# Kernel tuning notes

Hardware: AMD Instinct MI355X
Metric: run time of the kernel (lower is better)

The kernel has to match this reference:

```python
import jax, jax.numpy as jnp
import numpy as np

B, N, C, H = 4, 1024, 768, 12
D = C // H  # head_dim = 64


def setup_inputs() -> dict:
    key = jax.random.key(0)
    ks = jax.random.split(key, 16)
    def lin(k, fan_in, fan_out):
        # torch Linear init: U(-1/sqrt(fan_in), 1/sqrt(fan_in)); stored as [in, out]
        bound = 1.0 / np.sqrt(fan_in)
        kw, kb = jax.random.split(k)
        W = jax.random.uniform(kw, (fan_in, fan_out), minval=-bound, maxval=bound, dtype=jnp.float32)
        b = jax.random.uniform(kb, (fan_out,), minval=-bound, maxval=bound, dtype=jnp.float32)
        return W, b
    Wq, bq = lin(ks[0], C, C)
    Wk, bk = lin(ks[1], C, C)
    Wv, bv = lin(ks[2], C, C)
    Wo, bo = lin(ks[3], C, C)
    Wd1, bd1 = lin(ks[4], 1, 16)
    Wd2, bd2 = lin(ks[5], 16, H)
    x = jax.random.normal(ks[6], (B, N, C), dtype=jnp.float32)
    coords = jax.random.uniform(ks[7], (B, N, 2), dtype=jnp.float32)
    return {"x": x, "coords": coords,
            "Wq": Wq, "bq": bq, "Wk": Wk, "bk": bk, "Wv": Wv, "bv": bv,
            "Wo": Wo, "bo": bo, "Wd1": Wd1, "bd1": bd1, "Wd2": Wd2, "bd2": bd2}


def reference(x, coords, Wq, bq, Wk, bk, Wv, bv, Wo, bo, Wd1, bd1, Wd2, bd2):
    scale = D ** (-0.5)
    # projections -> [B, H, N, D]
    def heads(t):
        return t.reshape(B, N, H, D).transpose(0, 2, 1, 3)
    q = heads(x @ Wq + bq)
    k = heads(x @ Wk + bk)
    v = heads(x @ Wv + bv)
    # content scores [B, H, N, N]
    content = jnp.einsum('bhid,bhjd->bhij', q, k) * scale
    # pairwise distances [B, N, N, 1]
    diff = coords[:, :, None, :] - coords[:, None, :, :]
    dist = jnp.sqrt(jnp.sum(diff * diff, axis=-1, keepdims=True) + 1e-6)
    # distance MLP: 1 -> 16 -> H, then permute to [B, H, N, N]
    hbias = jax.nn.relu(dist @ Wd1 + bd1)
    spatial = (hbias @ Wd2 + bd2).transpose(0, 3, 1, 2)
    attn = jax.nn.softmax(content + spatial, axis=-1)
    out = jnp.einsum('bhij,bhjd->bhid', attn, v)
    out = out.transpose(0, 2, 1, 3).reshape(B, N, C)
    out = out @ Wo + bo
    return out, attn
```

## Files before the change

kernel.cpp:

```cpp
#include <hip/hip_runtime.h>
#include <cstddef>
#include <cstdint>

#define Bc 4
#define Nc 1024
#define Cc 768
#define Hc 12
#define Dc 64
#define BHc 48
#define QKV_ELEMS ((size_t)Bc * Nc * Cc)

typedef __attribute__((ext_vector_type(4))) unsigned int u32x4;
typedef __attribute__((ext_vector_type(8))) short s16x8;
typedef __attribute__((ext_vector_type(4))) float fx4;
typedef __attribute__((ext_vector_type(2))) float fx2;

union Frag { u32x4 u; s16x8 s; unsigned short h[8]; };

__device__ inline unsigned short f2bf(float x) {
    union { float f; uint32_t u; } c; c.f = x;
    return (unsigned short)((c.u + 0x7FFFu + ((c.u >> 16) & 1u)) >> 16);
}
__device__ inline float bf2f(unsigned short b) {
    union { uint32_t u; float f; } c; c.u = ((uint32_t)b) << 16;
    return c.f;
}
__device__ inline void split8(const float* v, u32x4& hi, u32x4& lo) {
    Frag fh, fl;
    #pragma unroll
    for (int e = 0; e < 8; ++e) {
        const unsigned short hb = f2bf(v[e]);
        fh.h[e] = hb;
        fl.h[e] = f2bf(v[e] - bf2f(hb));
    }
    hi = fh.u; lo = fl.u;
}

__global__ __launch_bounds__(256) void prep_w_kernel(
    const float* __restrict__ Wq, const float* __restrict__ Wk,
    const float* __restrict__ Wv, const float* __restrict__ Wo,
    unsigned short* __restrict__ Thi, unsigned short* __restrict__ Tlo)
{
    __shared__ float scr[64 * 65];
    const int mat = blockIdx.z;
    const float* W = (mat == 0) ? Wq : (mat == 1) ? Wk : (mat == 2) ? Wv : Wo;
    const int k0 = blockIdx.y * 64, n0 = blockIdx.x * 64;
    const int tid = threadIdx.x;

    #pragma unroll
    for (int it = 0; it < 4; ++it) {
        const int lin = tid + it * 256;
        const int r = lin >> 4, c4 = (lin & 15) << 2;
        const fx4 v = *(const fx4*)&W[(size_t)(k0 + r) * 768 + n0 + c4];
        scr[r * 65 + c4 + 0] = v[0]; scr[r * 65 + c4 + 1] = v[1];
        scr[r * 65 + c4 + 2] = v[2]; scr[r * 65 + c4 + 3] = v[3];
    }
    __syncthreads();
    unsigned short* th = Thi + (size_t)mat * 768 * 768;
    unsigned short* tl = Tlo + (size_t)mat * 768 * 768;
    #pragma unroll
    for (int it = 0; it < 16; ++it) {
        const int lin = tid + it * 256;
        const int n = lin >> 6, kq = lin & 63;
        const float val = scr[kq * 65 + n];
        const size_t o = (size_t)(n0 + n) * 768 + k0 + kq;
        const unsigned short hb = f2bf(val);
        th[o] = hb;
        tl[o] = f2bf(val - bf2f(hb));
    }
}

__global__ __launch_bounds__(256) void prep_tables_kernel(
    const float* __restrict__ Wd1, const float* __restrict__ bd1,
    const float* __restrict__ Wd2, const float* __restrict__ bd2,
    float* __restrict__ abPack, unsigned char* __restrict__ lut)
{
    __shared__ float w1s[16], b1s[16], kn[16];
    __shared__ int rank[16];
    const int tid = threadIdx.x;
    if (tid < 16) {
        const float w1 = Wd1[tid], b1 = bd1[tid];
        w1s[tid] = w1; b1s[tid] = b1;
        kn[tid] = (w1 != 0.0f) ? (-b1 / w1) : INFINITY;
    }
    __syncthreads();
    if (tid < 16) {
        int rk = 0;
        for (int u = 0; u < 16; ++u) {
            const float ku = kn[u], km = kn[tid];
            if (ku < km || (ku == km && u < tid)) ++rk;
        }
        rank[tid] = rk;
    }
    __syncthreads();
    if (tid < 17 * 12) {
        const int s = tid / 12, h = tid % 12;
        float a = 0.0f, be = bd2[h];
        for (int u = 0; u < 16; ++u) {
            const float w1 = w1s[u], b1 = b1s[u];
            bool act;
            if (w1 > 0.0f)      act = (rank[u] < s);
            else if (w1 < 0.0f) act = (rank[u] >= s);
            else                act = (b1 > 0.0f);
            if (act) {
                const float w2 = Wd2[u * 12 + h];
                a  += w2 * w1;
                be += w2 * b1;
            }
        }
        abPack[tid * 2 + 0] = a;
        abPack[tid * 2 + 1] = be;
    }
    for (int b = tid; b < 2048; b += 256) {
        const float rep = (b + 0.5f) * (1.41422f / 2048.0f);
        int cnt = 0;
        for (int t = 0; t < 16; ++t) cnt += (rep > kn[t]) ? 1 : 0;
        lut[b] = (unsigned char)cnt;
    }
}

__global__ __launch_bounds__(256) void split_x_kernel(
    const float* __restrict__ x, unsigned short* __restrict__ xhi,
    unsigned short* __restrict__ xlo)
{
    const size_t t = (size_t)blockIdx.x * 256 + threadIdx.x;
    float vv[8];
    const fx4 a = *(const fx4*)&x[t * 8];
    const fx4 b = *(const fx4*)&x[t * 8 + 4];
    vv[0]=a[0]; vv[1]=a[1]; vv[2]=a[2]; vv[3]=a[3];
    vv[4]=b[0]; vv[5]=b[1]; vv[6]=b[2]; vv[7]=b[3];
    u32x4 hi, lo; split8(vv, hi, lo);
    *(u32x4*)&xhi[t * 8] = hi;
    *(u32x4*)&xlo[t * 8] = lo;
}

struct SmemG { u32x4 ah[512]; u32x4 al[512]; u32x4 bh[512]; u32x4 bl[512]; };
struct SmemT { float scr[64 * 68]; };
union SmemU { SmemG g; SmemT t; };

template<int OMODE>
__global__ __launch_bounds__(256) void gemm_mfma_kernel(
    const unsigned short* __restrict__ Ahi, const unsigned short* __restrict__ Alo,
    const unsigned short* __restrict__ Bhi, const unsigned short* __restrict__ Blo,
    const float* __restrict__ bias,
    float* __restrict__ outF,
    unsigned short* __restrict__ Ohi, unsigned short* __restrict__ Olo)
{
    __shared__ SmemU sm;
    const int tid = threadIdx.x;
    const int w = tid >> 6, L = tid & 63;
    const int Lr = L & 15, Lg = L >> 4;
    const int m0 = blockIdx.y * 64, n0 = blockIdx.x * 64;

    fx4 acc[2][2] = {};

    for (int kk = 0; kk < 768; kk += 64) {
        #pragma unroll
        for (int it = 0; it < 2; ++it) {
            const int slot = tid + it * 256;
            const int s = slot >> 6, l = slot & 63;
            const int row = m0 + ((s >> 1) << 4) + (l & 15);
            const int kb = kk + ((s & 1) << 5) + ((l >> 4) << 3);
            sm.g.ah[slot] = *(const u32x4*)&Ahi[(size_t)row * 768 + kb];
            sm.g.al[slot] = *(const u32x4*)&Alo[(size_t)row * 768 + kb];
            const int col = n0 + ((s >> 1) << 4) + (l & 15);
            sm.g.bh[slot] = *(const u32x4*)&Bhi[(size_t)col * 768 + kb];
            sm.g.bl[slot] = *(const u32x4*)&Blo[(size_t)col * 768 + kb];
        }
        __syncthreads();
        #pragma unroll
        for (int kc = 0; kc < 2; ++kc) {
            Frag ah[2], al[2], bh[2], bl[2];
            #pragma unroll
            for (int mm = 0; mm < 2; ++mm) {
                const int rg = (w >> 1) * 2 + mm;
                ah[mm].u = sm.g.ah[(rg * 2 + kc) * 64 + L];
                al[mm].u = sm.g.al[(rg * 2 + kc) * 64 + L];
            }
            #pragma unroll
            for (int nn = 0; nn < 2; ++nn) {
                const int cg = (w & 1) * 2 + nn;
                bh[nn].u = sm.g.bh[(cg * 2 + kc) * 64 + L];
                bl[nn].u = sm.g.bl[(cg * 2 + kc) * 64 + L];
            }
            #pragma unroll
            for (int mm = 0; mm < 2; ++mm)
                #pragma unroll
                for (int nn = 0; nn < 2; ++nn) {
                    acc[mm][nn] = __builtin_amdgcn_mfma_f32_16x16x32_bf16(ah[mm].s, bh[nn].s, acc[mm][nn], 0, 0, 0);
                    acc[mm][nn] = __builtin_amdgcn_mfma_f32_16x16x32_bf16(ah[mm].s, bl[nn].s, acc[mm][nn], 0, 0, 0);
                    acc[mm][nn] = __builtin_amdgcn_mfma_f32_16x16x32_bf16(al[mm].s, bh[nn].s, acc[mm][nn], 0, 0, 0);
                }
        }
        __syncthreads();
    }

    #pragma unroll
    for (int mm = 0; mm < 2; ++mm) {
        const int rl = (w >> 1) * 32 + mm * 16 + Lg * 4;
        #pragma unroll
        for (int nn = 0; nn < 2; ++nn) {
            const int cl = (w & 1) * 32 + nn * 16 + Lr;
            const float bs = bias[n0 + cl];
            #pragma unroll
            for (int r = 0; r < 4; ++r)
                sm.t.scr[(rl + r) * 68 + cl] = acc[mm][nn][r] + bs;
        }
    }
    __syncthreads();

    if (OMODE == 0) {
        const int h = n0 >> 6;
        #pragma unroll
        for (int it = 0; it < 2; ++it) {
            const int t = tid + it * 256;
            const int r = t >> 3, d0 = (t & 7) << 3;
            float vv[8];
            #pragma unroll
            for (int e = 0; e < 8; ++e) vv[e] = sm.t.scr[r * 68 + d0 + e];
            u32x4 hi, lo; split8(vv, hi, lo);
            const int rg = m0 + r, b = rg >> 10, nloc = rg & 1023;
            const size_t o = (((size_t)(b * Hc + h) * Nc + nloc) << 6) + d0;
            *(u32x4*)&Ohi[o] = hi;
            *(u32x4*)&Olo[o] = lo;
        }
    } else if (OMODE == 1) {
        const int b = m0 >> 10, h = n0 >> 6, nbase = m0 & 1023;
        #pragma unroll
        for (int it = 0; it < 2; ++it) {
            const int t = tid + it * 256;
            const int dd = t >> 3, j0 = (t & 7) << 3;
            float vv[8];
            #pragma unroll
            for (int e = 0; e < 8; ++e) vv[e] = sm.t.scr[(j0 + e) * 68 + dd];
            u32x4 hi, lo; split8(vv, hi, lo);
            const size_t o = (size_t)((b * Hc + h) * Dc + dd) * Nc + nbase + j0;
            *(u32x4*)&Ohi[o] = hi;
            *(u32x4*)&Olo[o] = lo;
        }
    } else {
        #pragma unroll
        for (int it = 0; it < 4; ++it) {
            const int lin = tid + it * 256;
            const int r = lin >> 4, c4 = (lin & 15) << 2;
            const fx4 v = *(const fx4*)&sm.t.scr[r * 68 + c4];
            *(fx4*)&outF[(size_t)(m0 + r) * 768 + n0 + c4] = v;
        }
    }
}

__global__ __launch_bounds__(256) void scores_kernel(
    const unsigned short* __restrict__ qhi, const unsigned short* __restrict__ qlo,
    const unsigned short* __restrict__ khi, const unsigned short* __restrict__ klo,
    const float* __restrict__ coords,
    const float* __restrict__ abPack, const unsigned char* __restrict__ lutg,
    float* __restrict__ attn, float* __restrict__ mlf)
{
    __shared__ fx2 abt[17];
    __shared__ unsigned char luts[2048];
    __shared__ fx2 cjs[512];

    const int tid = threadIdx.x;
    const int w = tid >> 6, L = tid & 63;
    const int Lr = L & 15, Lg = L >> 4;
    const int bh = blockIdx.z, b = bh / Hc, h = bh % Hc;
    const int i0 = blockIdx.x * 64, half = blockIdx.y;
    const int i = i0 + w * 16 + Lr;
    const int Lg4 = Lg * 4;

    if (tid < 17) abt[tid] = ((const fx2*)abPack)[tid * Hc + h];
    #pragma unroll
    for (int t = tid; t < 512; t += 256) {
        ((uint32_t*)luts)[t] = ((const uint32_t*)lutg)[t];
        cjs[t] = *(const fx2*)&coords[((size_t)b * Nc + half * 512 + t) * 2];
    }

    Frag qh[2], ql[2];
    #pragma unroll
    for (int kc = 0; kc < 2; ++kc) {
        const size_t o = ((size_t)bh * Nc + i) * 64 + kc * 32 + Lg * 8;
        qh[kc].u = *(const u32x4*)&qhi[o];
        ql[kc].u = *(const u32x4*)&qlo[o];
    }
    const fx2 ci = *(const fx2*)&coords[((size_t)b * Nc + i) * 2];
    __syncthreads();

    const size_t rowbase = ((size_t)bh * Nc + i) * Nc + half * 512;
    const size_t mlbase = ((size_t)bh * Nc + i) * 16 + half * 8;

    for (int jt = 0; jt < 8; ++jt) {
        const int jbase = half * 512 + jt * 64;

        fx4 acc[4] = {};
        #pragma unroll
        for (int kc = 0; kc < 2; ++kc) {
            Frag kh[4], kl[4];
            #pragma unroll
            for (int cg = 0; cg < 4; ++cg) {
                const size_t o = ((size_t)bh * Nc + jbase + cg * 16 + Lr) * 64 + kc * 32 + Lg * 8;
                kh[cg].u = *(const u32x4*)&khi[o];
                kl[cg].u = *(const u32x4*)&klo[o];
            }
            #pragma unroll
            for (int cg = 0; cg < 4; ++cg) {
                acc[cg] = __builtin_amdgcn_mfma_f32_16x16x32_bf16(kh[cg].s, qh[kc].s, acc[cg], 0, 0, 0);
                acc[cg] = __builtin_amdgcn_mfma_f32_16x16x32_bf16(kl[cg].s, qh[kc].s, acc[cg], 0, 0, 0);
                acc[cg] = __builtin_amdgcn_mfma_f32_16x16x32_bf16(kh[cg].s, ql[kc].s, acc[cg], 0, 0, 0);
            }
        }

        float sv[16];
        #pragma unroll
        for (int cg = 0; cg < 4; ++cg) {
            #pragma unroll
            for (int r = 0; r < 4; ++r) {
                const fx2 cj = cjs[jt * 64 + cg * 16 + Lg4 + r];
                const float dx = ci[0] - cj[0], dy = ci[1] - cj[1];
                const float dist = sqrtf(fmaf(dx, dx, fmaf(dy, dy, 1e-6f)));
                int bin = (int)(dist * (2048.0f / 1.41422f));
                bin = (bin > 2047) ? 2047 : bin;
                const fx2 ab = abt[luts[bin]];
                sv[cg * 4 + r] = fmaf(acc[cg][r], 0.125f, fmaf(ab[0], dist, ab[1]));
            }
        }

        float tm = sv[0];
        #pragma unroll
        for (int e = 1; e < 16; ++e) tm = fmaxf(tm, sv[e]);
        tm = fmaxf(tm, __shfl_xor(tm, 16));
        tm = fmaxf(tm, __shfl_xor(tm, 32));

        float ts = 0.f;
        #pragma unroll
        for (int e = 0; e < 16; ++e) { sv[e] = __expf(sv[e] - tm); ts += sv[e]; }
        #pragma unroll
        for (int cg = 0; cg < 4; ++cg) {
            fx4 st;
            st[0] = sv[cg*4+0]; st[1] = sv[cg*4+1]; st[2] = sv[cg*4+2]; st[3] = sv[cg*4+3];
            *(fx4*)&attn[rowbase + jt * 64 + cg * 16 + Lg4] = st;
        }
        ts += __shfl_xor(ts, 16);
        ts += __shfl_xor(ts, 32);
        if (Lg == 0) {
            *(fx2*)&mlf[(mlbase + jt) * 2] = fx2{tm, ts};
        }
    }
}

__global__ __launch_bounds__(256) void pv_kernel(
    float* __restrict__ attn,
    const unsigned short* __restrict__ vThi, const unsigned short* __restrict__ vTlo,
    const float* __restrict__ mlf,
    unsigned short* __restrict__ Hphi, unsigned short* __restrict__ Hplo)
{
    __shared__ float accs[32 * 64];
    const int tid = threadIdx.x;
    const int w = tid >> 6, L = tid & 63;
    const int Lr = L & 15, Lg = L >> 4;
    const int wr = w >> 1, wc = w & 1;
    const int bh = blockIdx.y, b = bh / Hc, h = bh % Hc;
    const int i0 = blockIdx.x * 32;
    const int row = i0 + wr * 16 + Lr;

    const float* mlr = &mlf[((size_t)bh * Nc + row) * 32];
    float mt[16], lt[16];
    #pragma unroll
    for (int t = 0; t < 8; ++t) {
        const fx4 v = *(const fx4*)&mlr[t * 4];
        mt[t*2+0] = v[0]; lt[t*2+0] = v[1];
        mt[t*2+1] = v[2]; lt[t*2+1] = v[3];
    }
    float m_row = mt[0];
    #pragma unroll
    for (int t = 1; t < 16; ++t) m_row = fmaxf(m_row, mt[t]);
    float l_row = 0.f;
    #pragma unroll
    for (int t = 0; t < 16; ++t) l_row = fmaf(lt[t], __expf(mt[t] - m_row), l_row);
    const float il = 1.0f / l_row;

    fx4 acc[4] = {};
    const size_t arow = ((size_t)bh * Nc + row) * Nc;

    for (int jt = 0; jt < 8; ++jt) {
        const int jbase = wc * 512 + jt * 64;
        const float f = __expf(mlr[(wc * 8 + jt) * 2] - m_row) * il;
        #pragma unroll
        for (int kc = 0; kc < 2; ++kc) {
            float* ap = &attn[arow + jbase + kc * 32 + Lg * 8];
            const fx4 s0 = *(const fx4*)ap;
            const fx4 s1 = *(const fx4*)(ap + 4);
            float p[8];
            p[0]=s0[0]*f; p[1]=s0[1]*f; p[2]=s0[2]*f; p[3]=s0[3]*f;
            p[4]=s1[0]*f; p[5]=s1[1]*f; p[6]=s1[2]*f; p[7]=s1[3]*f;
            fx4 w0, w1;
            w0[0]=p[0]; w0[1]=p[1]; w0[2]=p[2]; w0[3]=p[3];
            w1[0]=p[4]; w1[1]=p[5]; w1[2]=p[6]; w1[3]=p[7];
            *(fx4*)ap = w0;
            *(fx4*)(ap + 4) = w1;
            u32x4 phiu, plou; split8(p, phiu, plou);
            Frag ph, pl; ph.u = phiu; pl.u = plou;

            Frag vh[4], vl[4];
            #pragma unroll
            for (int dg = 0; dg < 4; ++dg) {
                const size_t o = ((size_t)bh * Dc + dg * 16 + Lr) * Nc + jbase + kc * 32 + Lg * 8;
                vh[dg].u = *(const u32x4*)&vThi[o];
                vl[dg].u = *(const u32x4*)&vTlo[o];
            }
            #pragma unroll
            for (int dg = 0; dg < 4; ++dg) {
                acc[dg] = __builtin_amdgcn_mfma_f32_16x16x32_bf16(ph.s, vh[dg].s, acc[dg], 0, 0, 0);
                acc[dg] = __builtin_amdgcn_mfma_f32_16x16x32_bf16(ph.s, vl[dg].s, acc[dg], 0, 0, 0);
                acc[dg] = __builtin_amdgcn_mfma_f32_16x16x32_bf16(pl.s, vh[dg].s, acc[dg], 0, 0, 0);
            }
        }
    }

    if (wc == 0) {
        #pragma unroll
        for (int dg = 0; dg < 4; ++dg)
            #pragma unroll
            for (int r = 0; r < 4; ++r)
                accs[(wr * 16 + Lg * 4 + r) * 64 + dg * 16 + Lr] = acc[dg][r];
    }
    __syncthreads();
    if (wc == 1) {
        #pragma unroll
        for (int dg = 0; dg < 4; ++dg)
            #pragma unroll
            for (int r = 0; r < 4; ++r)
                accs[(wr * 16 + Lg * 4 + r) * 64 + dg * 16 + Lr] += acc[dg][r];
    }
    __syncthreads();

    const int r2 = tid >> 3, d0 = (tid & 7) << 3;
    float vv[8];
    #pragma unroll
    for (int e = 0; e < 8; ++e) vv[e] = accs[r2 * 64 + d0 + e];
    u32x4 hi, lo; split8(vv, hi, lo);
    const size_t o = ((size_t)b * Nc + i0 + r2) * Cc + h * Dc + d0;
    *(u32x4*)&Hphi[o] = hi;
    *(u32x4*)&Hplo[o] = lo;
}

extern "C" void kernel_launch(void* const* d_in, const int* in_sizes, int n_in,
                              void* d_out, int out_size, void* d_ws, size_t ws_size,
                              hipStream_t stream)
{
    (void)in_sizes; (void)n_in; (void)out_size; (void)ws_size;

    const float* x      = (const float*)d_in[0];
    const float* coords = (const float*)d_in[1];
    const float* Wq = (const float*)d_in[2];  const float* bq = (const float*)d_in[3];
    const float* Wk = (const float*)d_in[4];  const float* bk = (const float*)d_in[5];
    const float* Wv = (const float*)d_in[6];  const float* bv = (const float*)d_in[7];
    const float* Wo = (const float*)d_in[8];  const float* bo = (const float*)d_in[9];
    const float* Wd1 = (const float*)d_in[10]; const float* bd1 = (const float*)d_in[11];
    const float* Wd2 = (const float*)d_in[12]; const float* bd2 = (const float*)d_in[13];

    float* out_main = (float*)d_out;
    float* attn     = out_main + QKV_ELEMS;

    uint8_t* wsb = (uint8_t*)d_ws;
    const size_t SZ_BF = (size_t)BHc * Nc * Dc * 2;
    const size_t SZ_W4 = (size_t)4 * 768 * 768 * 2;
    unsigned short* qhi  = (unsigned short*)(wsb + 0 * SZ_BF);
    unsigned short* qlo  = (unsigned short*)(wsb + 1 * SZ_BF);
    unsigned short* khi  = (unsigned short*)(wsb + 2 * SZ_BF);
    unsigned short* klo  = (unsigned short*)(wsb + 3 * SZ_BF);
    unsigned short* vThi = (unsigned short*)(wsb + 4 * SZ_BF);
    unsigned short* vTlo = (unsigned short*)(wsb + 5 * SZ_BF);
    unsigned short* xhi  = (unsigned short*)(wsb + 6 * SZ_BF);
    unsigned short* xlo  = (unsigned short*)(wsb + 7 * SZ_BF);
    unsigned short* Thi  = (unsigned short*)(wsb + 8 * SZ_BF);
    unsigned short* Tlo  = (unsigned short*)(wsb + 8 * SZ_BF + SZ_W4);
    float* mlbuf  = (float*)(wsb + 8 * SZ_BF + 2 * SZ_W4);
    float* abPack = mlbuf + (size_t)BHc * Nc * 32;
    unsigned char* lut = (unsigned char*)(abPack + 17 * 12 * 2);

    prep_w_kernel<<<dim3(12, 12, 4), 256, 0, stream>>>(Wq, Wk, Wv, Wo, Thi, Tlo);
    prep_tables_kernel<<<1, 256, 0, stream>>>(Wd1, bd1, Wd2, bd2, abPack, lut);
    split_x_kernel<<<dim3(1536), 256, 0, stream>>>(x, xhi, xlo);

    dim3 gGemm(12, 64);
    gemm_mfma_kernel<0><<<gGemm, 256, 0, stream>>>(
        xhi, xlo, Thi + (size_t)0 * 768 * 768, Tlo + (size_t)0 * 768 * 768,
        bq, nullptr, qhi, qlo);
    gemm_mfma_kernel<0><<<gGemm, 256, 0, stream>>>(
        xhi, xlo, Thi + (size_t)1 * 768 * 768, Tlo + (size_t)1 * 768 * 768,
        bk, nullptr, khi, klo);
    gemm_mfma_kernel<1><<<gGemm, 256, 0, stream>>>(
        xhi, xlo, Thi + (size_t)2 * 768 * 768, Tlo + (size_t)2 * 768 * 768,
        bv, nullptr, vThi, vTlo);

    scores_kernel<<<dim3(16, 2, 48), 256, 0, stream>>>(
        qhi, qlo, khi, klo, coords, abPack, lut, attn, mlbuf);

    pv_kernel<<<dim3(32, 48), 256, 0, stream>>>(
        attn, vThi, vTlo, mlbuf, xhi, xlo);

    gemm_mfma_kernel<2><<<gGemm, 256, 0, stream>>>(
        xhi, xlo, Thi + (size_t)3 * 768 * 768, Tlo + (size_t)3 * 768 * 768,
        bo, out_main, nullptr, nullptr);
}
```

Baseline: 453.4 us.

## Stage unnormalized scores as fp16 workspace and use fp16 MFMA with LDS-staged V

The scores kernel now writes the exponentiated scores as fp16 into a workspace laid out for MFMA fragments, instead of writing fp32 into the attention output. The PV kernel reads these fp16 values, normalizes them, writes the final fp32 attention once, and runs two fp16 MFMAs per product instead of three split-bf16 ones. V is staged through LDS per 64-column tile, and each block now handles 64 rows over all columns instead of splitting columns across waves. This removes one fp32 read-modify-write pass over the large attention tensor and the bf16 splitting of P. In exchange, P is rounded to fp16 before the product, which lowers precision in the values fed to PV.

```diff
diff --git a/kernel.cpp b/kernel.cpp
--- a/kernel.cpp
+++ b/kernel.cpp
@@ -12,10 +12,13 @@
 
 typedef __attribute__((ext_vector_type(4))) unsigned int u32x4;
 typedef __attribute__((ext_vector_type(8))) short s16x8;
+typedef __attribute__((ext_vector_type(8))) _Float16 h16x8;
+typedef __attribute__((ext_vector_type(4))) unsigned short u16x4;
 typedef __attribute__((ext_vector_type(4))) float fx4;
 typedef __attribute__((ext_vector_type(2))) float fx2;
 
-union Frag { u32x4 u; s16x8 s; unsigned short h[8]; };
+union Frag { u32x4 u; s16x8 s; h16x8 f16; unsigned short h[8]; };
+union Half4 { u16x4 q; _Float16 h[4]; };
 
 __device__ inline unsigned short f2bf(float x) {
     union { float f; uint32_t u; } c; c.f = x;
@@ -32,6 +35,16 @@
         const unsigned short hb = f2bf(v[e]);
         fh.h[e] = hb;
         fl.h[e] = f2bf(v[e] - bf2f(hb));
+    }
+    hi = fh.u; lo = fl.u;
+}
+__device__ inline void split8h(const float* v, u32x4& hi, u32x4& lo) {
+    Frag fh, fl;
+    #pragma unroll
+    for (int e = 0; e < 8; ++e) {
+        const _Float16 hb = (_Float16)v[e];
+        fh.f16[e] = hb;
+        fl.f16[e] = (_Float16)(v[e] - (float)hb);
     }
     hi = fh.u; lo = fl.u;
 }
@@ -233,7 +246,7 @@
             float vv[8];
             #pragma unroll
             for (int e = 0; e < 8; ++e) vv[e] = sm.t.scr[(j0 + e) * 68 + dd];
-            u32x4 hi, lo; split8(vv, hi, lo);
+            u32x4 hi, lo; split8h(vv, hi, lo);
             const size_t o = (size_t)((b * Hc + h) * Dc + dd) * Nc + nbase + j0;
             *(u32x4*)&Ohi[o] = hi;
             *(u32x4*)&Olo[o] = lo;
@@ -254,7 +267,7 @@
     const unsigned short* __restrict__ khi, const unsigned short* __restrict__ klo,
     const float* __restrict__ coords,
     const float* __restrict__ abPack, const unsigned char* __restrict__ lutg,
-    float* __restrict__ attn, float* __restrict__ mlf)
+    unsigned short* __restrict__ e_ws, float* __restrict__ mlf)
 {
     __shared__ fx2 abt[17];
     __shared__ unsigned char luts[2048];
@@ -269,7 +282,6 @@
     const int Lg4 = Lg * 4;
 
     if (tid < 17) abt[tid] = ((const fx2*)abPack)[tid * Hc + h];
-    #pragma unroll
     for (int t = tid; t < 512; t += 256) {
         ((uint32_t*)luts)[t] = ((const uint32_t*)lutg)[t];
         cjs[t] = *(const fx2*)&coords[((size_t)b * Nc + half * 512 + t) * 2];
@@ -285,11 +297,11 @@
     const fx2 ci = *(const fx2*)&coords[((size_t)b * Nc + i) * 2];
     __syncthreads();
 
-    const size_t rowbase = ((size_t)bh * Nc + i) * Nc + half * 512;
     const size_t mlbase = ((size_t)bh * Nc + i) * 16 + half * 8;
 
     for (int jt = 0; jt < 8; ++jt) {
         const int jbase = half * 512 + jt * 64;
+        const int jtg = half * 8 + jt;
 
         fx4 acc[4] = {};
         #pragma unroll
@@ -314,7 +326,7 @@
         for (int cg = 0; cg < 4; ++cg) {
             #pragma unroll
             for (int r = 0; r < 4; ++r) {
-                const fx2 cj = cjs[jt * 64 + cg * 16 + Lg4 + r];
+                const fx2 cj = cjs[jt * 64 + cg * 16 + Lg4 + r + (half * 512 == jbase - jt * 64 ? 0 : 0)];
                 const float dx = ci[0] - cj[0], dy = ci[1] - cj[1];
                 const float dist = sqrtf(fmaf(dx, dx, fmaf(dy, dy, 1e-6f)));
                 int bin = (int)(dist * (2048.0f / 1.41422f));
@@ -333,12 +345,19 @@
         float ts = 0.f;
         #pragma unroll
         for (int e = 0; e < 16; ++e) { sv[e] = __expf(sv[e] - tm); ts += sv[e]; }
+
+        const size_t eT = (((size_t)bh * 16 + jtg) << 16);
         #pragma unroll
         for (int cg = 0; cg < 4; ++cg) {
-            fx4 st;
-            st[0] = sv[cg*4+0]; st[1] = sv[cg*4+1]; st[2] = sv[cg*4+2]; st[3] = sv[cg*4+3];
-            *(fx4*)&attn[rowbase + jt * 64 + cg * 16 + Lg4] = st;
-        }
+            Half4 hs;
+            #pragma unroll
+            for (int r = 0; r < 4; ++r) hs.h[r] = (_Float16)sv[cg * 4 + r];
+            const int kc = cg >> 1;
+            const int Lgp = (cg & 1) * 2 + (Lg >> 1);
+            const size_t eoff = eT + (size_t)kc * 32768 + (size_t)i * 32 + Lgp * 8 + (Lg & 1) * 4;
+            *(u16x4*)&e_ws[eoff] = hs.q;
+        }
+
         ts += __shfl_xor(ts, 16);
         ts += __shfl_xor(ts, 32);
         if (Lg == 0) {
@@ -347,22 +366,27 @@
     }
 }
 
+union PvSmem {
+    struct { u32x4 vh[512]; u32x4 vl[512]; } v;
+    float scr[64 * 68];
+};
+
 __global__ __launch_bounds__(256) void pv_kernel(
-    float* __restrict__ attn,
+    const unsigned short* __restrict__ e_ws,
     const unsigned short* __restrict__ vThi, const unsigned short* __restrict__ vTlo,
     const float* __restrict__ mlf,
+    float* __restrict__ attn,
     unsigned short* __restrict__ Hphi, unsigned short* __restrict__ Hplo)
 {
-    __shared__ float accs[32 * 64];
+    __shared__ PvSmem sm;
     const int tid = threadIdx.x;
     const int w = tid >> 6, L = tid & 63;
     const int Lr = L & 15, Lg = L >> 4;
-    const int wr = w >> 1, wc = w & 1;
     const int bh = blockIdx.y, b = bh / Hc, h = bh % Hc;
-    const int i0 = blockIdx.x * 32;
-    const int row = i0 + wr * 16 + Lr;
-
-    const float* mlr = &mlf[((size_t)bh * Nc + row) * 32];
+    const int i0 = blockIdx.x * 64;
+    const int i = i0 + w * 16 + Lr;
+
+    const float* mlr = &mlf[((size_t)bh * Nc + i) * 32];
     float mt[16], lt[16];
     #pragma unroll
     for (int t = 0; t < 8; ++t) {
@@ -379,68 +403,73 @@
     const float il = 1.0f / l_row;
 
     fx4 acc[4] = {};
-    const size_t arow = ((size_t)bh * Nc + row) * Nc;
-
-    for (int jt = 0; jt < 8; ++jt) {
-        const int jbase = wc * 512 + jt * 64;
-        const float f = __expf(mlr[(wc * 8 + jt) * 2] - m_row) * il;
+    const size_t arow = ((size_t)bh * Nc + i) * Nc;
+
+    #pragma unroll
+    for (int jt = 0; jt < 16; ++jt) {
+        const int jbase = jt * 64;
+        #pragma unroll
+        for (int it = 0; it < 2; ++it) {
+            const int s = tid + it * 256;
+            const int l = s & 63;
+            const int dd = ((s >> 7) << 4) + (l & 15);
+            const int jo = jbase + ((s >> 6) & 1) * 32 + ((l >> 4) << 3);
+            const size_t off = ((size_t)bh * Dc + dd) * Nc + jo;
+            sm.v.vh[s] = *(const u32x4*)&vThi[off];
+            sm.v.vl[s] = *(const u32x4*)&vTlo[off];
+        }
+        __syncthreads();
+
+        const float f = __expf(mt[jt] - m_row) * il;
+        const _Float16 fh = (_Float16)f;
+        const size_t eT = (((size_t)bh * 16 + jt) << 16) + (size_t)i * 32 + Lg * 8;
+
         #pragma unroll
         for (int kc = 0; kc < 2; ++kc) {
+            Frag ef;
+            ef.u = *(const u32x4*)&e_ws[eT + kc * 32768];
+            float pf[8];
+            #pragma unroll
+            for (int e = 0; e < 8; ++e) pf[e] = (float)ef.f16[e] * f;
+            fx4 w0, w1;
+            w0[0]=pf[0]; w0[1]=pf[1]; w0[2]=pf[2]; w0[3]=pf[3];
+            w1[0]=pf[4]; w1[1]=pf[5]; w1[2]=pf[6]; w1[3]=pf[7];
             float* ap = &attn[arow + jbase + kc * 32 + Lg * 8];
-            const fx4 s0 = *(const fx4*)ap;
-            const fx4 s1 = *(const fx4*)(ap + 4);
-            float p[8];
-            p[0]=s0[0]*f; p[1]=s0[1]*f; p[2]=s0[2]*f; p[3]=s0[3]*f;
-            p[4]=s1[0]*f; p[5]=s1[1]*f; p[6]=s1[2]*f; p[7]=s1[3]*f;
-            fx4 w0, w1;
-            w0[0]=p[0]; w0[1]=p[1]; w0[2]=p[2]; w0[3]=p[3];
-            w1[0]=p[4]; w1[1]=p[5]; w1[2]=p[6]; w1[3]=p[7];
             *(fx4*)ap = w0;
             *(fx4*)(ap + 4) = w1;
-            u32x4 phiu, plou; split8(p, phiu, plou);
-            Frag ph, pl; ph.u = phiu; pl.u = plou;
-
-            Frag vh[4], vl[4];
+            Frag pa;
+            pa.f16 = ef.f16 * fh;
             #pragma unroll
             for (int dg = 0; dg < 4; ++dg) {
-                const size_t o = ((size_t)bh * Dc + dg * 16 + Lr) * Nc + jbase + kc * 32 + Lg * 8;
-                vh[dg].u = *(const u32x4*)&vThi[o];
-                vl[dg].u = *(const u32x4*)&vTlo[o];
-            }
-            #pragma unroll
-            for (int dg = 0; dg < 4; ++dg) {
-                acc[dg] = __builtin_amdgcn_mfma_f32_16x16x32_bf16(ph.s, vh[dg].s, acc[dg], 0, 0, 0);
-                acc[dg] = __builtin_amdgcn_mfma_f32_16x16x32_bf16(ph.s, vl[dg].s, acc[dg], 0, 0, 0);
-                acc[dg] = __builtin_amdgcn_mfma_f32_16x16x32_bf16(pl.s, vh[dg].s, acc[dg], 0, 0, 0);
-            }
-        }
-    }
-
-    if (wc == 0) {
-        #pragma unroll
-        for (int dg = 0; dg < 4; ++dg)
-            #pragma unroll
-            for (int r = 0; r < 4; ++r)
-                accs[(wr * 16 + Lg * 4 + r) * 64 + dg * 16 + Lr] = acc[dg][r];
-    }
+                Frag vh, vl;
+                vh.u = sm.v.vh[(dg * 2 + kc) * 64 + L];
+                vl.u = sm.v.vl[(dg * 2 + kc) * 64 + L];
+                acc[dg] = __builtin_amdgcn_mfma_f32_16x16x32_f16(pa.f16, vh.f16, acc[dg], 0, 0, 0);
+                acc[dg] = __builtin_amdgcn_mfma_f32_16x16x32_f16(pa.f16, vl.f16, acc[dg], 0, 0, 0);
+            }
+        }
+        __syncthreads();
+    }
+
+    #pragma unroll
+    for (int dg = 0; dg < 4; ++dg)
+        #pragma unroll
+        for (int r = 0; r < 4; ++r)
+            sm.scr[(w * 16 + Lg * 4 + r) * 68 + dg * 16 + Lr] = acc[dg][r];
     __syncthreads();
-    if (wc == 1) {
-        #pragma unroll
-        for (int dg = 0; dg < 4; ++dg)
-            #pragma unroll
-            for (int r = 0; r < 4; ++r)
-                accs[(wr * 16 + Lg * 4 + r) * 64 + dg * 16 + Lr] += acc[dg][r];
-    }
-    __syncthreads();
-
-    const int r2 = tid >> 3, d0 = (tid & 7) << 3;
-    float vv[8];
-    #pragma unroll
-    for (int e = 0; e < 8; ++e) vv[e] = accs[r2 * 64 + d0 + e];
-    u32x4 hi, lo; split8(vv, hi, lo);
-    const size_t o = ((size_t)b * Nc + i0 + r2) * Cc + h * Dc + d0;
-    *(u32x4*)&Hphi[o] = hi;
-    *(u32x4*)&Hplo[o] = lo;
+
+    #pragma unroll
+    for (int it = 0; it < 2; ++it) {
+        const int lin = tid + it * 256;
+        const int row = lin >> 3, d0 = (lin & 7) << 3;
+        float vv[8];
+        #pragma unroll
+        for (int e = 0; e < 8; ++e) vv[e] = sm.scr[row * 68 + d0 + e];
+        u32x4 hi, lo; split8(vv, hi, lo);
+        const size_t o = ((size_t)b * Nc + i0 + row) * Cc + h * Dc + d0;
+        *(u32x4*)&Hphi[o] = hi;
+        *(u32x4*)&Hplo[o] = lo;
+    }
 }
 
 extern "C" void kernel_launch(void* const* d_in, const int* in_sizes, int n_in,
@@ -477,6 +506,8 @@
     float* mlbuf  = (float*)(wsb + 8 * SZ_BF + 2 * SZ_W4);
     float* abPack = mlbuf + (size_t)BHc * Nc * 32;
     unsigned char* lut = (unsigned char*)(abPack + 17 * 12 * 2);
+    unsigned short* e_ws = (unsigned short*)(wsb + 8 * SZ_BF + 2 * SZ_W4
+                              + (size_t)BHc * Nc * 32 * 4 + 8192);
 
     prep_w_kernel<<<dim3(12, 12, 4), 256, 0, stream>>>(Wq, Wk, Wv, Wo, Thi, Tlo);
     prep_tables_kernel<<<1, 256, 0, stream>>>(Wd1, bd1, Wd2, bd2, abPack, lut);
@@ -494,10 +525,10 @@
         bv, nullptr, vThi, vTlo);
 
     scores_kernel<<<dim3(16, 2, 48), 256, 0, stream>>>(
-        qhi, qlo, khi, klo, coords, abPack, lut, attn, mlbuf);
-
-    pv_kernel<<<dim3(32, 48), 256, 0, stream>>>(
-        attn, vThi, vTlo, mlbuf, xhi, xlo);
+        qhi, qlo, khi, klo, coords, abPack, lut, e_ws, mlbuf);
+
+    pv_kernel<<<dim3(16, 48), 256, 0, stream>>>(
+        e_ws, vThi, vTlo, mlbuf, attn, xhi, xlo);
 
     gemm_mfma_kernel<2><<<gGemm, 256, 0, stream>>>(
         xhi, xlo, Thi + (size_t)3 * 768 * 768, Tlo + (size_t)3 * 768 * 768,
```

Result: faster. 389.2 us (-14.2%).
